# Kernel tuning notes

Hardware: AMD Instinct MI355X
Metric: run time of the kernel (lower is better)

Reference implementation:

```python
import jax, jax.numpy as jnp
import numpy as np

G = 4          # deformable groups (from offset_and_mask_dim = 3*4*3*3)
K = 9          # 3x3 kernel points
GN_GROUPS = 16 # GroupNorm groups as in DyHead


def conv2d(x, w, stride=1, pad=1, groups=1):
    return jax.lax.conv_general_dilated(
        x, w, (stride, stride), [(pad, pad), (pad, pad)],
        dimension_numbers=('NCHW', 'OIHW', 'NCHW'),
        feature_group_count=groups)


def dw_conv(x, w, scale, bias):
    # YOLO Conv with g=in_channels: depthwise 3x3 + folded BN + SiLU
    C = x.shape[1]
    y = conv2d(x, w, groups=C)
    y = y * scale[None, :, None, None] + bias[None, :, None, None]
    return y * jax.nn.sigmoid(y)


def offset_mask_conv(x, w, b):
    # Conv2d(C, 108, 3, padding=1, groups=4)
    return conv2d(x, w, groups=G) + b[None, :, None, None]


def split_offset_mask(om, use_softmax):
    # om: (N,108,H,W) -> offset (N,H,W,G,K,2) in pixels (dy,dx), mask (N,H,W,G,K)
    N, _, H, W = om.shape
    om = om.transpose(0, 2, 3, 1)
    offset = om[..., :2 * G * K].reshape(N, H, W, G, K, 2)
    m = om[..., 2 * G * K:].reshape(N, H, W, G, K)
    mask = jax.nn.softmax(m, axis=-1) if use_softmax else jax.nn.sigmoid(m)
    return offset, mask


def group_norm(x, gamma, beta, eps=1e-5):
    N, C, H, W = x.shape
    xg = x.reshape(N, GN_GROUPS, C // GN_GROUPS, H, W)
    mu = xg.mean((2, 3, 4), keepdims=True)
    var = xg.var((2, 3, 4), keepdims=True)
    xg = (xg - mu) * jax.lax.rsqrt(var + eps)
    return xg.reshape(N, C, H, W) * gamma[None, :, None, None] + beta[None, :, None, None]


def dcnv3_sample(x, offset, mask, stride):
    # DCNv3 core: group-wise deformable 3x3 bilinear sampling, zero padding.
    # x: (N,C,H,W); offset: (N,Ho,Wo,G,K,2); mask: (N,Ho,Wo,G,K) -> (N,C,Ho,Wo)
    N, C, H, W = x.shape
    Cg = C // G
    Ho, Wo = offset.shape[1], offset.shape[2]
    xg = x.transpose(0, 2, 3, 1).reshape(N, H, W, G, Cg)
    kk = jnp.arange(3, dtype=x.dtype) - 1.0
    ky = jnp.repeat(kk, 3)  # (9,)
    kx = jnp.tile(kk, 3)
    base_y = (jnp.arange(Ho, dtype=x.dtype) * stride)[None, :, None, None, None]
    base_x = (jnp.arange(Wo, dtype=x.dtype) * stride)[None, None, :, None, None]
    py = base_y + ky + offset[..., 0]   # (N,Ho,Wo,G,K)
    px = base_x + kx + offset[..., 1]
    y0 = jnp.floor(py)
    x0 = jnp.floor(px)
    wy = py - y0
    wx = px - x0
    y0i = y0.astype(jnp.int32)
    x0i = x0.astype(jnp.int32)
    n_idx = jnp.arange(N)[:, None, None, None, None]
    g_idx = jnp.arange(G)[None, None, None, :, None]
    acc = jnp.zeros((N, Ho, Wo, G, Cg), x.dtype)
    for dy in (0, 1):
        for dx in (0, 1):
            yi = y0i + dy
            xi = x0i + dx
            w = (wy if dy else 1.0 - wy) * (wx if dx else 1.0 - wx)
            valid = (yi >= 0) & (yi < H) & (xi >= 0) & (xi < W)
            w = w * valid.astype(x.dtype) * mask
            v = xg[n_idx, jnp.clip(yi, 0, H - 1), jnp.clip(xi, 0, W - 1), g_idx]  # (N,Ho,Wo,G,K,Cg)
            acc = acc + jnp.einsum('nhwgk,nhwgkc->nhwgc', w, v)
    return acc.reshape(N, Ho, Wo, C).transpose(0, 3, 1, 2)


def up_bilinear_ac(x, Ho, Wo):
    # bilinear, align_corners=True
    N, C, H, W = x.shape
    def coords(out, size):
        c = jnp.arange(out, dtype=jnp.float32) * ((size - 1) / max(out - 1, 1))
        i0 = jnp.floor(c).astype(jnp.int32)
        i1 = jnp.minimum(i0 + 1, size - 1)
        return i0, i1, (c - i0).astype(x.dtype)
    y0, y1, wy = coords(Ho, H)
    xc0, xc1, wx = coords(Wo, W)
    t = x[:, :, y0, :] * (1.0 - wy)[None, None, :, None] + x[:, :, y1, :] * wy[None, None, :, None]
    return t[:, :, :, xc0] * (1.0 - wx) + t[:, :, :, xc1] * wx


def scale_attn(f, w, b):
    # AdaptiveAvgPool2d(1) -> Conv 1x1 (C->1) -> ReLU -> HSigmoid(bias=3, divisor=6)
    y = f.mean((2, 3))                      # (N,C)
    a = jax.nn.relu(y @ w.T + b)            # (N,1)
    a = jnp.clip((a + 3.0) / 6.0, 0.0, 1.0)
    return f * a[:, :, None, None]


def dyrelu(f, w1, b1_, w2, b2_):
    # DyReLU with K2=True, use_bias=True, lambda_a=2, init_a=[1,0], init_b=[0,0]
    y = f.mean((2, 3))                      # (N,C)
    h = jax.nn.relu(y @ w1.T + b1_)
    z = jnp.clip(h @ w2.T + b2_ + 3.0, 0.0, 6.0) / 6.0  # h_sigmoid
    a1, b1, a2, b2 = jnp.split(z, 4, axis=1)
    a1 = (a1 - 0.5) * 2.0 + 1.0
    a2 = (a2 - 0.5) * 2.0
    b1 = b1 - 0.5
    b2 = b2 - 0.5
    bc = lambda t: t[:, :, None, None]
    return jnp.maximum(f * bc(a1) + bc(b1), f * bc(a2) + bc(b2))


def _forward(x0, x1, x2,
             dw_w_h, dw_s_h, dw_b_h, dw_w_m, dw_s_m, dw_b_m, dw_w_l, dw_s_l, dw_b_l,
             off_w, off_b,
             gn_g_h, gn_b_h, gn_g_m, gn_b_m, gn_g_l, gn_b_l,
             sa_w, sa_b, fc1_w, fc1_b, fc2_w, fc2_b):
    xs = [x0, x1, x2]
    outs = []
    for lvl in range(3):
        x = xs[lvl]
        mid_ = dw_conv(x, dw_w_m, dw_s_m, dw_b_m)
        off, msk = split_offset_mask(offset_mask_conv(mid_, off_w, off_b), use_softmax=False)
        mid_feat = group_norm(dcnv3_sample(x, off, msk, 1), gn_g_m, gn_b_m)
        sum_feat = scale_attn(mid_feat, sa_w, sa_b)
        n_lvls = 1
        if lvl > 0:
            xl = xs[lvl - 1]
            low_ = dw_conv(xl, dw_w_l, dw_s_l, dw_b_l)
            off, msk = split_offset_mask(offset_mask_conv(low_, off_w, off_b), use_softmax=True)
            off = off[:, ::2, ::2]   # stride-2 output grid
            msk = msk[:, ::2, ::2]
            low_feat = group_norm(dcnv3_sample(xl, off, msk, 2), gn_g_l, gn_b_l)
            sum_feat = sum_feat + scale_attn(low_feat, sa_w, sa_b)
            n_lvls += 1
        if lvl < 2:
            xh = xs[lvl + 1]
            high_ = dw_conv(xh, dw_w_h, dw_s_h, dw_b_h)
            off, msk = split_offset_mask(offset_mask_conv(high_, off_w, off_b), use_softmax=True)
            high_feat = group_norm(dcnv3_sample(xh, off, msk, 1), gn_g_h, gn_b_h)
            high_feat = up_bilinear_ac(high_feat, x.shape[2], x.shape[3])
            sum_feat = sum_feat + scale_attn(high_feat, sa_w, sa_b)
            n_lvls += 1
        outs.append(dyrelu(sum_feat / n_lvls, fc1_w, fc1_b, fc2_w, fc2_b))
    return tuple(outs)


def setup_inputs() -> dict:
    key = jax.random.key(0)
    ks = jax.random.split(key, 32)
    N, C = 4, 256
    f32 = jnp.float32
    nrm = lambda k, shape, s=1.0: jax.random.normal(k, shape, f32) * s
    inp = {
        'x0': nrm(ks[0], (N, C, 80, 80)),
        'x1': nrm(ks[1], (N, C, 40, 40)),
        'x2': nrm(ks[2], (N, C, 20, 20)),
        'dw_w_h': nrm(ks[3], (C, 1, 3, 3), 0.1),
        'dw_s_h': 1.0 + nrm(ks[4], (C,), 0.1),
        'dw_b_h': nrm(ks[5], (C,), 0.1),
        'dw_w_m': nrm(ks[6], (C, 1, 3, 3), 0.1),
        'dw_s_m': 1.0 + nrm(ks[7], (C,), 0.1),
        'dw_b_m': nrm(ks[8], (C,), 0.1),
        'dw_w_l': nrm(ks[9], (C, 1, 3, 3), 0.1),
        'dw_s_l': 1.0 + nrm(ks[10], (C,), 0.1),
        'dw_b_l': nrm(ks[11], (C,), 0.1),
        'off_w': nrm(ks[12], (108, C // G, 3, 3), 0.1),
        'off_b': nrm(ks[13], (108,), 0.1),
        'gn_g_h': 1.0 + nrm(ks[14], (C,), 0.1),
        'gn_b_h': nrm(ks[15], (C,), 0.1),
        'gn_g_m': 1.0 + nrm(ks[16], (C,), 0.1),
        'gn_b_m': nrm(ks[17], (C,), 0.1),
        'gn_g_l': 1.0 + nrm(ks[18], (C,), 0.1),
        'gn_b_l': nrm(ks[19], (C,), 0.1),
        'sa_w': nrm(ks[20], (1, C), 0.05),
        'sa_b': nrm(ks[21], (1,), 0.05),
        'fc1_w': nrm(ks[22], (C // 4, C), 0.05),
        'fc1_b': nrm(ks[23], (C // 4,), 0.05),
        'fc2_w': nrm(ks[24], (4 * C, C // 4), 0.05),
        'fc2_b': nrm(ks[25], (4 * C,), 0.1),
    }
    return inp


def reference(x0, x1, x2,
              dw_w_h, dw_s_h, dw_b_h, dw_w_m, dw_s_m, dw_b_m, dw_w_l, dw_s_l, dw_b_l,
              off_w, off_b,
              gn_g_h, gn_b_h, gn_g_m, gn_b_m, gn_g_l, gn_b_l,
              sa_w, sa_b, fc1_w, fc1_b, fc2_w, fc2_b):
    return _forward(x0, x1, x2,
                    dw_w_h, dw_s_h, dw_b_h, dw_w_m, dw_s_m, dw_b_m, dw_w_l, dw_s_l, dw_b_l,
                    off_w, off_b,
                    gn_g_h, gn_b_h, gn_g_m, gn_b_m, gn_g_l, gn_b_l,
                    sa_w, sa_b, fc1_w, fc1_b, fc2_w, fc2_b)
```

## Files before the change

kernel.cpp:

```cpp
#include <hip/hip_runtime.h>
#include <hip/hip_bf16.h>

#define C_ 256
#define G_ 4

typedef __attribute__((ext_vector_type(8))) short bf16x8;
typedef __attribute__((ext_vector_type(4))) float f32x4;

static __device__ __forceinline__ unsigned short f2bf(float x) {
    __hip_bfloat16 h = __float2bfloat16(x);
    return *(unsigned short*)&h;
}
static __device__ __forceinline__ float bf2f(unsigned short u) {
    return __uint_as_float((unsigned)u << 16);
}
static __device__ __forceinline__ float4 bf4(ushort4 u) {
    float4 r;
    r.x = bf2f(u.x);
    r.y = bf2f(u.y);
    r.z = bf2f(u.z);
    r.w = bf2f(u.w);
    return r;
}

static __device__ __forceinline__ float upw(int y, int Hr, int Hf, float sys) {
    float inv = 1.f / sys;
    int lo = max(0, (int)((y - 1) * inv) - 1);
    int hi = min(Hf - 1, (int)((y + 1) * inv) + 1);
    float w = 0.f;
    for (int o = lo; o <= hi; o++) {
        float sy = o * sys;
        int y0 = (int)sy;
        float fy = sy - y0;
        int y1 = min(y0 + 1, Hr - 1);
        if (y0 == y) w += 1.f - fy;
        if (y1 == y) w += fy;
    }
    return w;
}

__global__ void k_prep(const float* __restrict__ off_w, const float* __restrict__ dwh,
                       const float* __restrict__ dwm, const float* __restrict__ dwl,
                       unsigned short* __restrict__ wmf, float* __restrict__ dwt,
                       float* __restrict__ zeros, float* __restrict__ rep) {
    int i = blockIdx.x * 256 + threadIdx.x;
    const int NWM = 4 * 32 * 576;
    if (i < NWM) {
        int g = i / (32 * 576), rem = i % (32 * 576);
        int ol = rem / 576, kk = rem % 576;
        int tap = kk / 64, ic = kk % 64;
        float v = (ol < 27) ? off_w[((size_t)((g * 27 + ol) * 64 + ic)) * 9 + tap] : 0.f;
        wmf[i] = f2bf(v);
    }
    int j = i - NWM;
    if (j >= 0 && j < 3 * 2304) {
        int which = j / 2304, rem = j % 2304;
        int t = rem / 256, c = rem % 256;
        const float* src = (which == 0) ? dwh : (which == 1) ? dwm : dwl;
        dwt[j] = src[c * 9 + t];
    }
    int z = i - NWM - 3 * 2304;
    if (z >= 0 && z < 896) zeros[z] = 0.f;
    int z2 = z - 896;
    if (z2 >= 0 && z2 < 4 * 7168) rep[z2] = 0.f;
}

struct TrP {
    const float* x[3];
    unsigned short* xtb[3];
    int H[3];
    int W[3];
    int wtc[3];
    int blk[4];
};

__global__ __launch_bounds__(256) void k_transpose_b(TrP P) {
    __shared__ float tile[32][33];
    int b = blockIdx.x;
    int f = (b >= P.blk[1]) + (b >= P.blk[2]);
    int l = b - P.blk[f];
    int H = P.H[f], W = P.W[f], wtc = P.wtc[f];
    int nh = l / wtc, wtile = l - nh * wtc;
    int n = nh / H, h = nh % H;
    int w0 = wtile * 32, c0 = blockIdx.y * 32;
    const float* x = P.x[f];
    unsigned short* xtb = P.xtb[f];
    int tid = threadIdx.x;
    int i = tid / 32, j = tid % 32;
#pragma unroll
    for (int r = 0; r < 4; r++) {
        int c = c0 + i + r * 8;
        int w = w0 + j;
        tile[i + r * 8][j] = (w < W) ? x[((size_t)(n * C_ + c) * H + h) * W + w] : 0.f;
    }
    __syncthreads();
    int wj = tid >> 4, ci2 = (tid & 15) * 2;
#pragma unroll
    for (int r = 0; r < 2; r++) {
        int w = w0 + wj + r * 16;
        if (w < W) {
            ushort2 o;
            o.x = f2bf(tile[ci2][wj + r * 16]);
            o.y = f2bf(tile[ci2 + 1][wj + r * 16]);
            *(ushort2*)(xtb + ((size_t)(n * H + h) * W + w) * C_ + c0 + ci2) = o;
        }
    }
}

struct DwP {
    const unsigned short* xtb[7];
    unsigned short* out[7];
    const float* wdt[7];
    const float* sc[7];
    const float* bi[7];
    int H[7];
    int W[7];
    int blk[8];
};

__global__ __launch_bounds__(256) void k_dw_silu_b(DwP P) {
    int b = blockIdx.x;
    int f = (b >= P.blk[1]) + (b >= P.blk[2]) + (b >= P.blk[3]) + (b >= P.blk[4]) +
            (b >= P.blk[5]) + (b >= P.blk[6]);
    int H = P.H[f], W = P.W[f];
    const unsigned short* xtbf = P.xtb[f];
    unsigned short* outf = P.out[f];
    const float* wdt = P.wdt[f];
    int tid = threadIdx.x;
    int wv = tid >> 6, lane = tid & 63;
    int half = lane >> 5, l5 = lane & 31;
    int ch8 = l5 << 3;
    int pix = (b - P.blk[f]) * 8 + wv * 2 + half;
    int w = pix % W, h = (pix / W) % H, n = pix / (W * H);
    const float4 sA = *(const float4*)(P.sc[f] + ch8);
    const float4 sB = *(const float4*)(P.sc[f] + ch8 + 4);
    const float4 bA = *(const float4*)(P.bi[f] + ch8);
    const float4 bB = *(const float4*)(P.bi[f] + ch8 + 4);
    const unsigned short* xb = xtbf + (size_t)n * H * W * C_ + ch8;
    float4 accA = {0.f, 0.f, 0.f, 0.f}, accB = {0.f, 0.f, 0.f, 0.f};
#pragma unroll
    for (int t = 0; t < 9; t++) {
        int hh = h + t / 3 - 1, ww = w + t % 3 - 1;
        if (hh >= 0 && hh < H && ww >= 0 && ww < W) {
            bf16x8 xv = *(const bf16x8*)(xb + (size_t)(hh * W + ww) * C_);
            float4 wa = *(const float4*)(wdt + t * 256 + ch8);
            float4 wb = *(const float4*)(wdt + t * 256 + ch8 + 4);
            accA.x += wa.x * bf2f((unsigned short)xv[0]);
            accA.y += wa.y * bf2f((unsigned short)xv[1]);
            accA.z += wa.z * bf2f((unsigned short)xv[2]);
            accA.w += wa.w * bf2f((unsigned short)xv[3]);
            accB.x += wb.x * bf2f((unsigned short)xv[4]);
            accB.y += wb.y * bf2f((unsigned short)xv[5]);
            accB.z += wb.z * bf2f((unsigned short)xv[6]);
            accB.w += wb.w * bf2f((unsigned short)xv[7]);
        }
    }
    float y0 = accA.x * sA.x + bA.x, y1 = accA.y * sA.y + bA.y;
    float y2 = accA.z * sA.z + bA.z, y3 = accA.w * sA.w + bA.w;
    float y4 = accB.x * sB.x + bB.x, y5 = accB.y * sB.y + bB.y;
    float y6 = accB.z * sB.z + bB.z, y7 = accB.w * sB.w + bB.w;
    y0 = y0 / (1.f + __expf(-y0));
    y1 = y1 / (1.f + __expf(-y1));
    y2 = y2 / (1.f + __expf(-y2));
    y3 = y3 / (1.f + __expf(-y3));
    y4 = y4 / (1.f + __expf(-y4));
    y5 = y5 / (1.f + __expf(-y5));
    y6 = y6 / (1.f + __expf(-y6));
    y7 = y7 / (1.f + __expf(-y7));
    uint4 ov;
    ov.x = (unsigned)f2bf(y0) | ((unsigned)f2bf(y1) << 16);
    ov.y = (unsigned)f2bf(y2) | ((unsigned)f2bf(y3) << 16);
    ov.z = (unsigned)f2bf(y4) | ((unsigned)f2bf(y5) << 16);
    ov.w = (unsigned)f2bf(y6) | ((unsigned)f2bf(y7) << 16);
    *(uint4*)(outf + (size_t)pix * C_ + ch8) = ov;
}

struct OmP7 {
    const unsigned short* dwb[7];
    float* om[7];
    int Hs[7], Ws[7], Wo[7], HoWo[7];
    int ss[7];
    int ths[7], tws[7];
    int SR[7], SC[7], Msc[7];
    int nz[7], Mnz[7];
    int blk[8];
};

__global__ __launch_bounds__(256) void k_offmask_b(OmP7 P,
                                                   const unsigned short* __restrict__ wmf) {
    __shared__ __align__(16) char smem[22032];
    unsigned short* patch = (unsigned short*)smem;
    float* omv = (float*)smem;

    int tid = threadIdx.x;
    int wv = tid >> 6, lane = tid & 63;
    int n16 = lane & 15, q = lane >> 4;
    int b = blockIdx.x;
    int f = (b >= P.blk[1]) + (b >= P.blk[2]) + (b >= P.blk[3]) + (b >= P.blk[4]) +
            (b >= P.blk[5]) + (b >= P.blk[6]);
    int l = b - P.blk[f];
    int n = (l >> 2) & 3, g = l & 3;
    int tile = l >> 4;
    int nz = P.nz[f];
    int ty = (tile * P.Mnz[f]) >> 16;
    int tz = tile - ty * nz;
    int ss = P.ss[f], ths = P.ths[f], tws = P.tws[f];
    int TW = 1 << tws;
    int SR = P.SR[f], SC = P.SC[f], Msc = P.Msc[f];
    int NV = SR * SC;
    int Hs = P.Hs[f], Ws = P.Ws[f], Wo = P.Wo[f], HoWo = P.HoWo[f];
    int ho0 = ty << ths, wo0 = tz << tws;
    int hs0 = (ho0 << ss) - 1, ws0 = (wo0 << ss) - 1;
    const unsigned short* dwb = P.dwb[f];
    float* om = P.om[f];

    for (int idx = tid; idx < NV * 8; idx += 256) {
        int pp = idx >> 3;
        int c8 = (idx & 7) << 3;
        int pq = (pp * Msc) >> 16;
        int hh = hs0 + pq, ww = ws0 + (pp - pq * SC);
        uint4 v = {0u, 0u, 0u, 0u};
        if (hh >= 0 && hh < Hs && ww >= 0 && ww < Ws)
            v = *(const uint4*)(dwb + ((size_t)(n * Hs + hh) * Ws + ww) * C_ + g * 64 + c8);
        *(uint4*)(patch + pp * 72 + c8) = v;
    }
    __syncthreads();

    int bchan = q << 3;
    const unsigned short* wg = wmf + (size_t)g * 32 * 576;
    int TP = 1 << (ths + tws);
    int sc1 = SC, sc2 = SC * 2;

    if (TP == 64) {
        int p = wv * 16 + n16;
        int pr = p >> tws, pc = p & (TW - 1);
        int pixbase = (pr << ss) * SC + (pc << ss);
        f32x4 a0 = {0.f, 0.f, 0.f, 0.f}, a1 = {0.f, 0.f, 0.f, 0.f};
#pragma unroll
        for (int kk = 0; kk < 18; kk++) {
            int tap = kk >> 1;
            int ic0 = (kk & 1) << 5;
            int tr = tap / 3, tc = tap % 3;
            int ppix = pixbase + (tr == 0 ? 0 : (tr == 1 ? sc1 : sc2)) + tc;
            bf16x8 bb = *(const bf16x8*)(patch + ppix * 72 + ic0 + bchan);
            bf16x8 wa0 = *(const bf16x8*)(wg + (size_t)n16 * 576 + kk * 32 + bchan);
            bf16x8 wa1 = *(const bf16x8*)(wg + (size_t)(16 + n16) * 576 + kk * 32 + bchan);
            a0 = __builtin_amdgcn_mfma_f32_16x16x32_bf16(wa0, bb, a0, 0, 0, 0);
            a1 = __builtin_amdgcn_mfma_f32_16x16x32_bf16(wa1, bb, a1, 0, 0, 0);
        }
        __syncthreads();
#pragma unroll
        for (int r = 0; r < 4; r++) {
            int ol0 = q * 4 + r;
            omv[p * 28 + ol0] = a0[r];
            int ol1 = 16 + q * 4 + r;
            if (ol1 < 28) omv[p * 28 + ol1] = a1[r];
        }
    } else {
        int NT = TP >> 3;
        int t = wv;
        bool active = t < NT;
        int ntile = t >> 1, mtile = t & 1;
        int p = ntile * 16 + n16;
        int pr = p >> tws, pc = p & (TW - 1);
        int pixbase = (pr << ss) * SC + (pc << ss);
        f32x4 acc = {0.f, 0.f, 0.f, 0.f};
        if (active) {
#pragma unroll
            for (int kk = 0; kk < 18; kk++) {
                int tap = kk >> 1;
                int ic0 = (kk & 1) << 5;
                int tr = tap / 3, tc = tap % 3;
                int ppix = pixbase + (tr == 0 ? 0 : (tr == 1 ? sc1 : sc2)) + tc;
                bf16x8 bb = *(const bf16x8*)(patch + ppix * 72 + ic0 + bchan);
                bf16x8 wa = *(const bf16x8*)(wg + (size_t)(mtile * 16 + n16) * 576 +
                                             kk * 32 + bchan);
                acc = __builtin_amdgcn_mfma_f32_16x16x32_bf16(wa, bb, acc, 0, 0, 0);
            }
        }
        __syncthreads();
        if (active) {
#pragma unroll
            for (int r = 0; r < 4; r++) {
                int ol = mtile * 16 + q * 4 + r;
                if (ol < 28) omv[p * 28 + ol] = acc[r];
            }
        }
    }
    __syncthreads();

    float* omg = om + ((size_t)(g * 4 + n)) * HoWo * 28;
    for (int idx = tid; idx < TP * 7; idx += 256) {
        int p = (idx * 9363) >> 16;
        int c4 = idx - p * 7;
        int ho = ho0 + (p >> tws), wo = wo0 + (p & (TW - 1));
        int pixn = ho * Wo + wo;
        *(float4*)(omg + (size_t)pixn * 28 + c4 * 4) = *(float4*)(omv + p * 28 + c4 * 4);
    }
}

struct SmP {
    const unsigned short* xtb[7];
    const float* om[7];
    unsigned short* raw[7];
    float* stats[7];
    float* rsum[7];
    int Hs[7];
    int Ws[7];
    int Wo[7];
    int HoWo[7];
    int stride[7];
    int softmax[7];
    int up[7];
    int Hf[7];
    int Wf2[7];
    float sys[7];
    float sxs[7];
    int blk[8];
};

__global__ __launch_bounds__(256) void k_sample_b(SmP P, const float* __restrict__ bias) {
    int tid = threadIdx.x;
    int wv = tid >> 6, lane = tid & 63;
    int halfp = lane >> 5, l5 = lane & 31;
    int g = l5 >> 3;
    int ch8 = l5 << 3;
    int nb = gridDim.x;
    int per = nb >> 3, rem = nb & 7;
    int xcd = blockIdx.x & 7, bi = blockIdx.x >> 3;
    int logical = xcd * per + min(xcd, rem) + bi;
    int f = (logical >= P.blk[1]) + (logical >= P.blk[2]) + (logical >= P.blk[3]) +
            (logical >= P.blk[4]) + (logical >= P.blk[5]) + (logical >= P.blk[6]);
    const unsigned short* xtb = P.xtb[f];
    const float* om = P.om[f];
    unsigned short* raw = P.raw[f];
    float* stats = P.stats[f];
    float* rsum = P.rsum[f] + (blockIdx.x & 3) * 7168;
    int Hs = P.Hs[f], Ws = P.Ws[f], Wo = P.Wo[f], HoWo = P.HoWo[f];
    int stride = P.stride[f], softmax = P.softmax[f];
    int upf = P.up[f];
    int pix0 = (logical - P.blk[f]) * 8;
    int n = pix0 / HoWo;
    int pixn0 = pix0 - n * HoWo;

    __shared__ float lom[8 * 112];
    __shared__ float lb[108];
    __shared__ float sm[32][9];
    __shared__ float4 lw[288];
    __shared__ ushort4 li[288];
    __shared__ float lstat[32];
    __shared__ float lsum[8][256];
    __shared__ float wup[8];

    if (tid < 224) {
        int gc = tid / 56, r2 = tid % 56;
        int pp = r2 / 7, c4 = r2 % 7;
        float4 v = *(const float4*)(om + ((size_t)(gc * 4 + n) * HoWo + pixn0 + pp) * 28 +
                                    c4 * 4);
        ((float4*)lom)[pp * 28 + gc * 7 + c4] = v;
    }
    if (tid < 108) lb[tid] = bias[tid];
    if (tid < 32) lstat[tid] = 0.f;
    __syncthreads();

    if (tid < 32) {
        int pp = tid >> 2, gs = tid & 3;
        float mv[9];
#pragma unroll
        for (int k = 0; k < 9; k++) {
            int ch = 72 + gs * 9 + k;
            int gc = ch / 27;
            mv[k] = lom[pp * 112 + gc * 28 + (ch - gc * 27)] + lb[ch];
        }
        if (softmax) {
            float mx = -1e30f;
#pragma unroll
            for (int k = 0; k < 9; k++) mx = fmaxf(mx, mv[k]);
            float ssum = 0.f;
#pragma unroll
            for (int k = 0; k < 9; k++) {
                mv[k] = __expf(mv[k] - mx);
                ssum += mv[k];
            }
            float inv = 1.f / ssum;
#pragma unroll
            for (int k = 0; k < 9; k++) sm[tid][k] = mv[k] * inv;
        } else {
#pragma unroll
            for (int k = 0; k < 9; k++) sm[tid][k] = 1.f / (1.f + __expf(-mv[k]));
        }
    }
    if (tid < 8) {
        float w = 1.f;
        if (upf) {
            int Ho = HoWo / Wo;
            int pixn = pixn0 + tid;
            int ho = pixn / Wo, wo = pixn - ho * Wo;
            w = upw(ho, Ho, P.Hf[f], P.sys[f]) * upw(wo, Wo, P.Wf2[f], P.sxs[f]);
        }
        wup[tid] = w;
    }
    __syncthreads();

    for (int idx = tid; idx < 288; idx += 256) {
        int pg = idx / 9, k = idx % 9;
        int pp = pg >> 2, gs = pg & 3;
        int chy = gs * 18 + 2 * k, chx = chy + 1;
        int gcy = chy / 27, gcx = chx / 27;
        float oy = lom[pp * 112 + gcy * 28 + (chy - gcy * 27)] + lb[chy];
        float ox = lom[pp * 112 + gcx * 28 + (chx - gcx * 27)] + lb[chx];
        int pixn = pixn0 + pp;
        int ho = pixn / Wo, wo = pixn % Wo;
        float py = (float)(ho * stride + k / 3 - 1) + oy;
        float px = (float)(wo * stride + k % 3 - 1) + ox;
        float y0f = floorf(py), x0f = floorf(px);
        int y0 = (int)y0f, x0 = (int)x0f;
        float wy = py - y0f, wx = px - x0f;
        int y1 = y0 + 1, x1 = x0 + 1;
        float v0y = (y0 >= 0 && y0 < Hs) ? 1.f : 0.f;
        float v1y = (y1 >= 0 && y1 < Hs) ? 1.f : 0.f;
        float v0x = (x0 >= 0 && x0 < Ws) ? 1.f : 0.f;
        float v1x = (x1 >= 0 && x1 < Ws) ? 1.f : 0.f;
        int y0c = min(max(y0, 0), Hs - 1), y1c = min(max(y1, 0), Hs - 1);
        int x0c = min(max(x0, 0), Ws - 1), x1c = min(max(x1, 0), Ws - 1);
        float m_ = sm[pg][k];
        float4 w4;
        w4.x = (1.f - wy) * (1.f - wx) * v0y * v0x * m_;
        w4.y = (1.f - wy) * wx * v0y * v1x * m_;
        w4.z = wy * (1.f - wx) * v1y * v0x * m_;
        w4.w = wy * wx * v1y * v1x * m_;
// ... 185 lines not shown
__global__ __launch_bounds__(256) void k_store_b(StP P, const float* __restrict__ coef,
                                                 const float* __restrict__ af) {
    __shared__ float tile[64][65];
    int b = blockIdx.x;
    int f = (b >= P.blk[1]) + (b >= P.blk[2]);
    int l = b - P.blk[f];
    int npt = P.npt[f], HW = P.HW[f], Wf = P.Wf[f], nf = P.nf[f];
    int n = l / (npt * 4);
    int r_ = l - n * (npt * 4);
    int pt = r_ >> 2;
    int c0 = (r_ & 3) * 64;
    float* out = P.out[f];
    const float* coefL = coef + f * 4096;
    const float* afL = af + f * 16;
    int tid = threadIdx.x;
    int lane16 = tid & 15, prow = tid >> 4;
    int ch4 = c0 + lane16 * 4;
    int gg = ch4 >> 4;
    float a0 = afL[n * 4 + 0], a1f = afL[n * 4 + 1], a2f = afL[n * 4 + 2];
    float4 ca1 = *(const float4*)(coefL + n * 1024 + 0 + ch4);
    float4 cb1 = *(const float4*)(coefL + n * 1024 + 256 + ch4);
    float4 ca2 = *(const float4*)(coefL + n * 1024 + 512 + ch4);
    float4 cb2 = *(const float4*)(coefL + n * 1024 + 768 + ch4);

    StF sA = P.ft[f][0], sB = P.ft[f][1], sC = P.ft[f][2];
    auto mkgb = [&](const StF& s, float4& ga, float4& be) {
        float s1 = s.stats[(n * 16 + gg) * 2], s2 = s.stats[(n * 16 + gg) * 2 + 1];
        float mu = s1 / s.cnt;
        float var = s2 / s.cnt - mu * mu;
        float rs = rsqrtf(var + 1e-5f);
        float4 gm = *(const float4*)(s.gamma + ch4);
        float4 bt = *(const float4*)(s.beta + ch4);
        ga.x = gm.x * rs; be.x = bt.x - mu * ga.x;
        ga.y = gm.y * rs; be.y = bt.y - mu * ga.y;
        ga.z = gm.z * rs; be.z = bt.z - mu * ga.z;
        ga.w = gm.w * rs; be.w = bt.w - mu * ga.w;
    };
    float4 gaA, beA, gaB, beB, gaC = {0, 0, 0, 0}, beC = {0, 0, 0, 0};
    mkgb(sA, gaA, beA);
    mkgb(sB, gaB, beB);
    if (nf > 2) mkgb(sC, gaC, beC);

    auto rdf = [&](const StF& s, int p) -> float4 {
        if (!s.up)
            return bf4(*(const ushort4*)(s.raw + ((size_t)n * HW + p) * C_ + ch4));
        int ho = p / Wf, wo = p - ho * Wf;
        float sy = ho * s.sys, sx = wo * s.sxs;
        int y0 = (int)sy, x0 = (int)sx;
        float fy = sy - y0, fx = sx - x0;
        int y1 = min(y0 + 1, s.Hr - 1), x1 = min(x0 + 1, s.Wr - 1);
        const unsigned short* rb = s.raw + (size_t)n * s.Hr * s.Wr * C_ + ch4;
        float4 v00 = bf4(*(const ushort4*)(rb + (size_t)(y0 * s.Wr + x0) * C_));
        float4 v01 = bf4(*(const ushort4*)(rb + (size_t)(y0 * s.Wr + x1) * C_));
        float4 v10 = bf4(*(const ushort4*)(rb + (size_t)(y1 * s.Wr + x0) * C_));
        float4 v11 = bf4(*(const ushort4*)(rb + (size_t)(y1 * s.Wr + x1) * C_));
        float4 v;
        v.x = (v00.x * (1.f - fy) + v10.x * fy) * (1.f - fx) + (v01.x * (1.f - fy) + v11.x * fy) * fx;
        v.y = (v00.y * (1.f - fy) + v10.y * fy) * (1.f - fx) + (v01.y * (1.f - fy) + v11.y * fy) * fx;
        v.z = (v00.z * (1.f - fy) + v10.z * fy) * (1.f - fx) + (v01.z * (1.f - fy) + v11.z * fy) * fx;
        v.w = (v00.w * (1.f - fy) + v10.w * fy) * (1.f - fx) + (v01.w * (1.f - fy) + v11.w * fy) * fx;
        return v;
    };

#pragma unroll
    for (int pass = 0; pass < 4; pass++) {
        int px = pass * 16 + prow;
        int p = pt * 64 + px;
        if (p < HW) {
            float4 vA = rdf(sA, p);
            float4 fv;
            fv.x = (vA.x * gaA.x + beA.x) * a0;
            fv.y = (vA.y * gaA.y + beA.y) * a0;
            fv.z = (vA.z * gaA.z + beA.z) * a0;
            fv.w = (vA.w * gaA.w + beA.w) * a0;
            float4 vB = rdf(sB, p);
            fv.x += (vB.x * gaB.x + beB.x) * a1f;
            fv.y += (vB.y * gaB.y + beB.y) * a1f;
            fv.z += (vB.z * gaB.z + beB.z) * a1f;
            fv.w += (vB.w * gaB.w + beB.w) * a1f;
            if (nf > 2) {
                float4 vC = rdf(sC, p);
                fv.x += (vC.x * gaC.x + beC.x) * a2f;
                fv.y += (vC.y * gaC.y + beC.y) * a2f;
                fv.z += (vC.z * gaC.z + beC.z) * a2f;
                fv.w += (vC.w * gaC.w + beC.w) * a2f;
            }
            int cr = lane16 * 4;
            tile[cr + 0][px] = fmaxf(fv.x * ca1.x + cb1.x, fv.x * ca2.x + cb2.x);
            tile[cr + 1][px] = fmaxf(fv.y * ca1.y + cb1.y, fv.y * ca2.y + cb2.y);
            tile[cr + 2][px] = fmaxf(fv.z * ca1.z + cb1.z, fv.z * ca2.z + cb2.z);
            tile[cr + 3][px] = fmaxf(fv.w * ca1.w + cb1.w, fv.w * ca2.w + cb2.w);
        }
    }
    __syncthreads();
#pragma unroll
    for (int wp = 0; wp < 4; wp++) {
        int row = wp * 16 + (tid >> 4);
        int px4 = (tid & 15) * 4;
        int p = pt * 64 + px4;
        if (p < HW) {
            float4 r;
            r.x = tile[row][px4 + 0];
            r.y = tile[row][px4 + 1];
            r.z = tile[row][px4 + 2];
            r.w = tile[row][px4 + 3];
            *(float4*)(out + (size_t)(n * C_ + c0 + row) * HW + p) = r;
        }
    }
}

extern "C" void kernel_launch(void* const* d_in, const int* in_sizes, int n_in,
                              void* d_out, int out_size, void* d_ws, size_t ws_size,
                              hipStream_t stream) {
    (void)in_sizes; (void)n_in; (void)out_size; (void)ws_size;
    const float* x0 = (const float*)d_in[0];
    const float* x1 = (const float*)d_in[1];
    const float* x2 = (const float*)d_in[2];
    const float* dw_w_h = (const float*)d_in[3];
    const float* dw_s_h = (const float*)d_in[4];
    const float* dw_b_h = (const float*)d_in[5];
    const float* dw_w_m = (const float*)d_in[6];
    const float* dw_s_m = (const float*)d_in[7];
    const float* dw_b_m = (const float*)d_in[8];
    const float* dw_w_l = (const float*)d_in[9];
    const float* dw_s_l = (const float*)d_in[10];
    const float* dw_b_l = (const float*)d_in[11];
    const float* off_w = (const float*)d_in[12];
    const float* off_b = (const float*)d_in[13];
    const float* gn_g_h = (const float*)d_in[14];
    const float* gn_b_h = (const float*)d_in[15];
    const float* gn_g_m = (const float*)d_in[16];
    const float* gn_b_m = (const float*)d_in[17];
    const float* gn_g_l = (const float*)d_in[18];
    const float* gn_b_l = (const float*)d_in[19];
    const float* sa_w = (const float*)d_in[20];
    const float* sa_b = (const float*)d_in[21];
    const float* fc1_w = (const float*)d_in[22];
    const float* fc1_b = (const float*)d_in[23];
    const float* fc2_w = (const float*)d_in[24];
    const float* fc2_b = (const float*)d_in[25];

    float* ws = (float*)d_ws;
    unsigned short* XTB0 = (unsigned short*)(ws + 0);
    unsigned short* XTB1 = (unsigned short*)(ws + 3276800);
    unsigned short* XTB2 = (unsigned short*)(ws + 4096000);
    float* SH = ws + 4300800;
    float* FINA = ws + 10854400;
    float* FINB = ws + 17408000;
    float* FINC = ws + 23961600;
    float* WMF = ws + 25600000;
    float* DWT = ws + 25636864;
    float* STATS = ws + 25643776;

    unsigned short* SHB = (unsigned short*)SH;
    unsigned short* FINAB = (unsigned short*)FINA;
    unsigned short* WMFB = (unsigned short*)WMF;

    float* out0 = (float*)d_out;
    float* out1 = out0 + 6553600;
    float* out2 = out0 + 8192000;

    float* OM_l0mid = out0;
    float* OM_l0high = out0 + 2867200;
    float* OM_l1mid = out0 + 3584000;
    float* OM_l1low = out0 + 4300800;
    float* OM_l1high = out1;
    float* OM_l2mid = out1 + 179200;
    float* OM_l2low = out1 + 358400;

    unsigned short* RAW_l0mid = (unsigned short*)SH;
    unsigned short* RAW_l0high = (unsigned short*)FINC;
    unsigned short* RAW_l1mid = (unsigned short*)FINB;
    unsigned short* RAW_l1low = (unsigned short*)(FINB + 1638400);
    unsigned short* RAW_l1high = (unsigned short*)(FINB + 3276800);
    unsigned short* RAW_l2mid = (unsigned short*)(FINB + 3686400);
    unsigned short* RAW_l2low = (unsigned short*)(FINB + 4096000);
    float* REP = FINB + 4505600;
    float* COEF = FINA;
    float* AF = FINA + 12288;

    const float SYS_L0H = (float)(39.0 / 79.0);
    const float SYS_L1H = (float)(19.0 / 39.0);

    k_prep<<<(4 * 32 * 576 + 6912 + 896 + 28672 + 255) / 256, 256, 0, stream>>>(
        off_w, dw_w_h, dw_w_m, dw_w_l, WMFB, DWT, STATS, REP);

    {
        TrP tp{};
        tp.x[0] = x0; tp.xtb[0] = XTB0; tp.H[0] = 80; tp.W[0] = 80; tp.wtc[0] = 3;
        tp.x[1] = x1; tp.xtb[1] = XTB1; tp.H[1] = 40; tp.W[1] = 40; tp.wtc[1] = 2;
        tp.x[2] = x2; tp.xtb[2] = XTB2; tp.H[2] = 20; tp.W[2] = 20; tp.wtc[2] = 1;
        tp.blk[0] = 0; tp.blk[1] = 960; tp.blk[2] = 1280; tp.blk[3] = 1360;
        k_transpose_b<<<dim3(1360, 8), 256, 0, stream>>>(tp);
    }

    unsigned short* DWB_x0mid = SHB;
    unsigned short* DWB_x0low = SHB + 6553600;
    unsigned short* DWB_x1high = FINAB;
    unsigned short* DWB_x1mid = FINAB + 1638400;
    unsigned short* DWB_x1low = FINAB + 3276800;
    unsigned short* DWB_x2high = FINAB + 4915200;
    unsigned short* DWB_x2mid = FINAB + 5324800;

    {
        DwP dp{};
        dp.xtb[0] = XTB0; dp.out[0] = DWB_x0mid;  dp.wdt[0] = DWT + 1 * 2304;
        dp.sc[0] = dw_s_m; dp.bi[0] = dw_b_m; dp.H[0] = 80; dp.W[0] = 80;
        dp.xtb[1] = XTB0; dp.out[1] = DWB_x0low;  dp.wdt[1] = DWT + 2 * 2304;
        dp.sc[1] = dw_s_l; dp.bi[1] = dw_b_l; dp.H[1] = 80; dp.W[1] = 80;
        dp.xtb[2] = XTB1; dp.out[2] = DWB_x1high; dp.wdt[2] = DWT + 0 * 2304;
        dp.sc[2] = dw_s_h; dp.bi[2] = dw_b_h; dp.H[2] = 40; dp.W[2] = 40;
        dp.xtb[3] = XTB1; dp.out[3] = DWB_x1mid;  dp.wdt[3] = DWT + 1 * 2304;
        dp.sc[3] = dw_s_m; dp.bi[3] = dw_b_m; dp.H[3] = 40; dp.W[3] = 40;
        dp.xtb[4] = XTB1; dp.out[4] = DWB_x1low;  dp.wdt[4] = DWT + 2 * 2304;
        dp.sc[4] = dw_s_l; dp.bi[4] = dw_b_l; dp.H[4] = 40; dp.W[4] = 40;
        dp.xtb[5] = XTB2; dp.out[5] = DWB_x2high; dp.wdt[5] = DWT + 0 * 2304;
        dp.sc[5] = dw_s_h; dp.bi[5] = dw_b_h; dp.H[5] = 20; dp.W[5] = 20;
        dp.xtb[6] = XTB2; dp.out[6] = DWB_x2mid;  dp.wdt[6] = DWT + 1 * 2304;
        dp.sc[6] = dw_s_m; dp.bi[6] = dw_b_m; dp.H[6] = 20; dp.W[6] = 20;
        dp.blk[0] = 0;    dp.blk[1] = 3200; dp.blk[2] = 6400; dp.blk[3] = 7200;
        dp.blk[4] = 8000; dp.blk[5] = 8800; dp.blk[6] = 9000; dp.blk[7] = 9200;
        k_dw_silu_b<<<9200, 256, 0, stream>>>(dp);
    }

    {
        OmP7 op{};
        auto setf = [&](int i, const unsigned short* dwb, float* om, int Hs, int Ws,
                        int Wo, int HoWo, int ss, int ths, int tws, int SR, int SC,
                        int nz) {
            op.dwb[i] = dwb; op.om[i] = om;
            op.Hs[i] = Hs; op.Ws[i] = Ws; op.Wo[i] = Wo; op.HoWo[i] = HoWo;
            op.ss[i] = ss; op.ths[i] = ths; op.tws[i] = tws;
            op.SR[i] = SR; op.SC[i] = SC; op.Msc[i] = (65536 + SC - 1) / SC;
            op.nz[i] = nz; op.Mnz[i] = (65536 + nz - 1) / nz;
        };
        setf(0, DWB_x0mid,  OM_l0mid,  80, 80, 80, 6400, 0, 3, 3, 10, 10, 10);
        setf(1, DWB_x1high, OM_l0high, 40, 40, 40, 1600, 0, 2, 3, 6,  10, 5);
        setf(2, DWB_x1mid,  OM_l1mid,  40, 40, 40, 1600, 0, 2, 3, 6,  10, 5);
        setf(3, DWB_x0low,  OM_l1low,  80, 80, 40, 1600, 1, 2, 3, 9,  17, 5);
        setf(4, DWB_x2high, OM_l1high, 20, 20, 20, 400,  0, 2, 2, 6,  6,  5);
        setf(5, DWB_x2mid,  OM_l2mid,  20, 20, 20, 400,  0, 2, 2, 6,  6,  5);
        setf(6, DWB_x1low,  OM_l2low,  40, 40, 20, 400,  1, 2, 2, 9,  9,  5);
        op.blk[0] = 0;    op.blk[1] = 1600; op.blk[2] = 2400; op.blk[3] = 3200;
        op.blk[4] = 4000; op.blk[5] = 4400; op.blk[6] = 4800; op.blk[7] = 5200;
        k_offmask_b<<<5200, 256, 0, stream>>>(op, WMFB);
    }

    {
        SmP sp{};
        auto setf = [&](int i, const unsigned short* xtb, const float* om,
                        unsigned short* raw, int slot, int Hs, int Ws, int Wo, int HoWo,
                        int stride, int softmax, int up, int Hf, int Wf2, float sys,
                        float sxs) {
            sp.xtb[i] = xtb; sp.om[i] = om; sp.raw[i] = raw;
            sp.stats[i] = STATS + slot * 128;
            sp.rsum[i] = REP + slot * 1024;
            sp.Hs[i] = Hs; sp.Ws[i] = Ws; sp.Wo[i] = Wo; sp.HoWo[i] = HoWo;
            sp.stride[i] = stride; sp.softmax[i] = softmax;
            sp.up[i] = up; sp.Hf[i] = Hf; sp.Wf2[i] = Wf2;
            sp.sys[i] = sys; sp.sxs[i] = sxs;
        };
        setf(0, XTB0, OM_l0mid,  RAW_l0mid,  0, 80, 80, 80, 6400, 1, 0, 0, 80, 80, 1.f, 1.f);
        setf(1, XTB1, OM_l0high, RAW_l0high, 1, 40, 40, 40, 1600, 1, 1, 1, 80, 80, SYS_L0H, SYS_L0H);
        setf(2, XTB1, OM_l1mid,  RAW_l1mid,  2, 40, 40, 40, 1600, 1, 0, 0, 40, 40, 1.f, 1.f);
        setf(3, XTB0, OM_l1low,  RAW_l1low,  3, 80, 80, 40, 1600, 2, 1, 0, 40, 40, 1.f, 1.f);
        setf(4, XTB2, OM_l1high, RAW_l1high, 4, 20, 20, 20, 400,  1, 1, 1, 40, 40, SYS_L1H, SYS_L1H);
        setf(5, XTB2, OM_l2mid,  RAW_l2mid,  5, 20, 20, 20, 400,  1, 0, 0, 20, 20, 1.f, 1.f);
        setf(6, XTB1, OM_l2low,  RAW_l2low,  6, 40, 40, 20, 400,  2, 1, 0, 20, 20, 1.f, 1.f);
        sp.blk[0] = 0;    sp.blk[1] = 3200; sp.blk[2] = 4000; sp.blk[3] = 4800;
        sp.blk[4] = 5600; sp.blk[5] = 5800; sp.blk[6] = 6000; sp.blk[7] = 6200;
        k_sample_b<<<6200, 256, 0, stream>>>(sp, off_b);
    }

    {
        CfP cp{};
        cp.nf[0] = 2; cp.inv_nl[0] = 0.5f;      cp.inv_hw[0] = 1.f / 6400.f;
        cp.nf[1] = 3; cp.inv_nl[1] = 1.f / 3.f; cp.inv_hw[1] = 1.f / 1600.f;
        cp.nf[2] = 2; cp.inv_nl[2] = 0.5f;      cp.inv_hw[2] = 1.f / 400.f;
        cp.ft[0][0] = {REP + 0 * 1024, STATS + 0 * 128, gn_g_m, gn_b_m, 102400.f};
        cp.ft[0][1] = {REP + 1 * 1024, STATS + 1 * 128, gn_g_h, gn_b_h, 25600.f};
        cp.ft[1][0] = {REP + 2 * 1024, STATS + 2 * 128, gn_g_m, gn_b_m, 25600.f};
        cp.ft[1][1] = {REP + 3 * 1024, STATS + 3 * 128, gn_g_l, gn_b_l, 25600.f};
        cp.ft[1][2] = {REP + 4 * 1024, STATS + 4 * 128, gn_g_h, gn_b_h, 6400.f};
        cp.ft[2][0] = {REP + 5 * 1024, STATS + 5 * 128, gn_g_m, gn_b_m, 6400.f};
        cp.ft[2][1] = {REP + 6 * 1024, STATS + 6 * 128, gn_g_l, gn_b_l, 6400.f};
        k_coef_b<<<12, 256, 0, stream>>>(cp, sa_w, sa_b, fc1_w, fc1_b, fc2_w, fc2_b,
                                         COEF, AF);
    }

    {
        StP st{};
        st.out[0] = out0; st.nf[0] = 2; st.HW[0] = 6400; st.Wf[0] = 80; st.npt[0] = 100;
        st.out[1] = out1; st.nf[1] = 3; st.HW[1] = 1600; st.Wf[1] = 40; st.npt[1] = 25;
        st.out[2] = out2; st.nf[2] = 2; st.HW[2] = 400;  st.Wf[2] = 20; st.npt[2] = 7;
        st.ft[0][0] = {RAW_l0mid,  STATS + 0 * 128, gn_g_m, gn_b_m, 102400.f, 0, 80, 80, 1.f, 1.f};
        st.ft[0][1] = {RAW_l0high, STATS + 1 * 128, gn_g_h, gn_b_h, 25600.f,  1, 40, 40, SYS_L0H, SYS_L0H};
        st.ft[1][0] = {RAW_l1mid,  STATS + 2 * 128, gn_g_m, gn_b_m, 25600.f,  0, 40, 40, 1.f, 1.f};
        st.ft[1][1] = {RAW_l1low,  STATS + 3 * 128, gn_g_l, gn_b_l, 25600.f,  0, 40, 40, 1.f, 1.f};
        st.ft[1][2] = {RAW_l1high, STATS + 4 * 128, gn_g_h, gn_b_h, 6400.f,   1, 20, 20, SYS_L1H, SYS_L1H};
        st.ft[2][0] = {RAW_l2mid,  STATS + 5 * 128, gn_g_m, gn_b_m, 6400.f,   0, 20, 20, 1.f, 1.f};
        st.ft[2][1] = {RAW_l2low,  STATS + 6 * 128, gn_g_l, gn_b_l, 6400.f,   0, 20, 20, 1.f, 1.f};
        st.blk[0] = 0; st.blk[1] = 1600; st.blk[2] = 2000; st.blk[3] = 2112;
        k_store_b<<<2112, 256, 0, stream>>>(st, COEF, AF);
    }
}
```

Baseline: 358.6 us.

## Fuse depthwise conv+SiLU into offset/mask conv via shared-memory halo patch

Removes the standalone depthwise conv + BN + SiLU kernel and its bf16 intermediate buffers. Each offset/mask block now loads a wider halo patch of the transposed input into shared memory and computes the depthwise output for its patch there, then runs the MFMA grouped conv on it. The work is split into two template instantiations, one for the stride-1 levels and one for the stride-2 levels, each sized for its patch. This saves a global write and read of seven intermediate maps, but recomputes the depthwise conv on overlapping halos and uses more shared memory per block, which could lower occupancy.

```diff
diff --git a/kernel.cpp b/kernel.cpp
--- a/kernel.cpp
+++ b/kernel.cpp
@@ -107,97 +107,31 @@
     }
 }
 
-struct DwP {
-    const unsigned short* xtb[7];
-    unsigned short* out[7];
-    const float* wdt[7];
-    const float* sc[7];
-    const float* bi[7];
-    int H[7];
-    int W[7];
-    int blk[8];
+struct OdP {
+    const unsigned short* xtb[5];
+    float* om[5];
+    const float* wdt[5];
+    const float* sc[5];
+    const float* bi[5];
+    int Hs[5], Ws[5], Wo[5], HoWo[5];
+    int ss[5], ths[5], tws[5];
+    int SR[5], SC[5], Msc[5], XC[5], Mxc[5];
+    int nz[5], Mnz[5];
+    int blk[6];
 };
 
-__global__ __launch_bounds__(256) void k_dw_silu_b(DwP P) {
-    int b = blockIdx.x;
-    int f = (b >= P.blk[1]) + (b >= P.blk[2]) + (b >= P.blk[3]) + (b >= P.blk[4]) +
-            (b >= P.blk[5]) + (b >= P.blk[6]);
-    int H = P.H[f], W = P.W[f];
-    const unsigned short* xtbf = P.xtb[f];
-    unsigned short* outf = P.out[f];
-    const float* wdt = P.wdt[f];
-    int tid = threadIdx.x;
-    int wv = tid >> 6, lane = tid & 63;
-    int half = lane >> 5, l5 = lane & 31;
-    int ch8 = l5 << 3;
-    int pix = (b - P.blk[f]) * 8 + wv * 2 + half;
-    int w = pix % W, h = (pix / W) % H, n = pix / (W * H);
-    const float4 sA = *(const float4*)(P.sc[f] + ch8);
-    const float4 sB = *(const float4*)(P.sc[f] + ch8 + 4);
-    const float4 bA = *(const float4*)(P.bi[f] + ch8);
-    const float4 bB = *(const float4*)(P.bi[f] + ch8 + 4);
-    const unsigned short* xb = xtbf + (size_t)n * H * W * C_ + ch8;
-    float4 accA = {0.f, 0.f, 0.f, 0.f}, accB = {0.f, 0.f, 0.f, 0.f};
-#pragma unroll
-    for (int t = 0; t < 9; t++) {
-        int hh = h + t / 3 - 1, ww = w + t % 3 - 1;
-        if (hh >= 0 && hh < H && ww >= 0 && ww < W) {
-            bf16x8 xv = *(const bf16x8*)(xb + (size_t)(hh * W + ww) * C_);
-            float4 wa = *(const float4*)(wdt + t * 256 + ch8);
-            float4 wb = *(const float4*)(wdt + t * 256 + ch8 + 4);
-            accA.x += wa.x * bf2f((unsigned short)xv[0]);
-            accA.y += wa.y * bf2f((unsigned short)xv[1]);
-            accA.z += wa.z * bf2f((unsigned short)xv[2]);
-            accA.w += wa.w * bf2f((unsigned short)xv[3]);
-            accB.x += wb.x * bf2f((unsigned short)xv[4]);
-            accB.y += wb.y * bf2f((unsigned short)xv[5]);
-            accB.z += wb.z * bf2f((unsigned short)xv[6]);
-            accB.w += wb.w * bf2f((unsigned short)xv[7]);
-        }
-    }
-    float y0 = accA.x * sA.x + bA.x, y1 = accA.y * sA.y + bA.y;
-    float y2 = accA.z * sA.z + bA.z, y3 = accA.w * sA.w + bA.w;
-    float y4 = accB.x * sB.x + bB.x, y5 = accB.y * sB.y + bB.y;
-    float y6 = accB.z * sB.z + bB.z, y7 = accB.w * sB.w + bB.w;
-    y0 = y0 / (1.f + __expf(-y0));
-    y1 = y1 / (1.f + __expf(-y1));
-    y2 = y2 / (1.f + __expf(-y2));
-    y3 = y3 / (1.f + __expf(-y3));
-    y4 = y4 / (1.f + __expf(-y4));
-    y5 = y5 / (1.f + __expf(-y5));
-    y6 = y6 / (1.f + __expf(-y6));
-    y7 = y7 / (1.f + __expf(-y7));
-    uint4 ov;
-    ov.x = (unsigned)f2bf(y0) | ((unsigned)f2bf(y1) << 16);
-    ov.y = (unsigned)f2bf(y2) | ((unsigned)f2bf(y3) << 16);
-    ov.z = (unsigned)f2bf(y4) | ((unsigned)f2bf(y5) << 16);
-    ov.w = (unsigned)f2bf(y6) | ((unsigned)f2bf(y7) << 16);
-    *(uint4*)(outf + (size_t)pix * C_ + ch8) = ov;
-}
-
-struct OmP7 {
-    const unsigned short* dwb[7];
-    float* om[7];
-    int Hs[7], Ws[7], Wo[7], HoWo[7];
-    int ss[7];
-    int ths[7], tws[7];
-    int SR[7], SC[7], Msc[7];
-    int nz[7], Mnz[7];
-    int blk[8];
-};
-
-__global__ __launch_bounds__(256) void k_offmask_b(OmP7 P,
-                                                   const unsigned short* __restrict__ wmf) {
-    __shared__ __align__(16) char smem[22032];
-    unsigned short* patch = (unsigned short*)smem;
-    float* omv = (float*)smem;
+template <int XPX, int PPX>
+__global__ __launch_bounds__(256) void k_offdw_b(OdP P,
+                                                 const unsigned short* __restrict__ wmf) {
+    __shared__ __align__(16) unsigned short xpatch[XPX * 72];
+    __shared__ __align__(16) unsigned short patch[PPX * 72];
+    float* omv = (float*)xpatch;
 
     int tid = threadIdx.x;
     int wv = tid >> 6, lane = tid & 63;
     int n16 = lane & 15, q = lane >> 4;
     int b = blockIdx.x;
-    int f = (b >= P.blk[1]) + (b >= P.blk[2]) + (b >= P.blk[3]) + (b >= P.blk[4]) +
-            (b >= P.blk[5]) + (b >= P.blk[6]);
+    int f = (b >= P.blk[1]) + (b >= P.blk[2]) + (b >= P.blk[3]) + (b >= P.blk[4]);
     int l = b - P.blk[f];
     int n = (l >> 2) & 3, g = l & 3;
     int tile = l >> 4;
@@ -207,22 +141,74 @@
     int ss = P.ss[f], ths = P.ths[f], tws = P.tws[f];
     int TW = 1 << tws;
     int SR = P.SR[f], SC = P.SC[f], Msc = P.Msc[f];
+    int XC = P.XC[f], Mxc = P.Mxc[f];
+    int XNV = (SR + 2) * XC;
     int NV = SR * SC;
     int Hs = P.Hs[f], Ws = P.Ws[f], Wo = P.Wo[f], HoWo = P.HoWo[f];
     int ho0 = ty << ths, wo0 = tz << tws;
     int hs0 = (ho0 << ss) - 1, ws0 = (wo0 << ss) - 1;
-    const unsigned short* dwb = P.dwb[f];
+    const unsigned short* xtb = P.xtb[f] + (size_t)n * Hs * Ws * C_ + g * 64;
     float* om = P.om[f];
+    const float* wdt = P.wdt[f] + g * 64;
+    const float* scp = P.sc[f] + g * 64;
+    const float* bip = P.bi[f] + g * 64;
+
+    for (int idx = tid; idx < XNV * 8; idx += 256) {
+        int pp = idx >> 3;
+        int c8 = (idx & 7) << 3;
+        int pq = (pp * Mxc) >> 16;
+        int hh = hs0 - 1 + pq, ww = ws0 - 1 + (pp - pq * XC);
+        uint4 v = {0u, 0u, 0u, 0u};
+        if (hh >= 0 && hh < Hs && ww >= 0 && ww < Ws)
+            v = *(const uint4*)(xtb + ((size_t)hh * Ws + ww) * C_ + c8);
+        *(uint4*)(xpatch + pp * 72 + c8) = v;
+    }
+    __syncthreads();
 
     for (int idx = tid; idx < NV * 8; idx += 256) {
         int pp = idx >> 3;
         int c8 = (idx & 7) << 3;
         int pq = (pp * Msc) >> 16;
-        int hh = hs0 + pq, ww = ws0 + (pp - pq * SC);
-        uint4 v = {0u, 0u, 0u, 0u};
-        if (hh >= 0 && hh < Hs && ww >= 0 && ww < Ws)
-            v = *(const uint4*)(dwb + ((size_t)(n * Hs + hh) * Ws + ww) * C_ + g * 64 + c8);
-        *(uint4*)(patch + pp * 72 + c8) = v;
+        int pr = pq, pc = pp - pq * SC;
+        int hh = hs0 + pr, ww = ws0 + pc;
+        uint4 ov = {0u, 0u, 0u, 0u};
+        if (hh >= 0 && hh < Hs && ww >= 0 && ww < Ws) {
+            float4 accA = {0.f, 0.f, 0.f, 0.f}, accB = {0.f, 0.f, 0.f, 0.f};
+#pragma unroll
+            for (int t = 0; t < 9; t++) {
+                int xr = pr + t / 3, xc = pc + t % 3;
+                bf16x8 xv = *(const bf16x8*)(xpatch + (xr * XC + xc) * 72 + c8);
+                float4 wa = *(const float4*)(wdt + t * 256 + c8);
+                float4 wb = *(const float4*)(wdt + t * 256 + c8 + 4);
+                accA.x += wa.x * bf2f((unsigned short)xv[0]);
+                accA.y += wa.y * bf2f((unsigned short)xv[1]);
+                accA.z += wa.z * bf2f((unsigned short)xv[2]);
+                accA.w += wa.w * bf2f((unsigned short)xv[3]);
+                accB.x += wb.x * bf2f((unsigned short)xv[4]);
+                accB.y += wb.y * bf2f((unsigned short)xv[5]);
+                accB.z += wb.z * bf2f((unsigned short)xv[6]);
+                accB.w += wb.w * bf2f((unsigned short)xv[7]);
+            }
+            float4 sa = *(const float4*)(scp + c8), sb = *(const float4*)(scp + c8 + 4);
+            float4 ba = *(const float4*)(bip + c8), bb = *(const float4*)(bip + c8 + 4);
+            float y0 = accA.x * sa.x + ba.x, y1 = accA.y * sa.y + ba.y;
+            float y2 = accA.z * sa.z + ba.z, y3 = accA.w * sa.w + ba.w;
+            float y4 = accB.x * sb.x + bb.x, y5 = accB.y * sb.y + bb.y;
+            float y6 = accB.z * sb.z + bb.z, y7 = accB.w * sb.w + bb.w;
+            y0 = y0 / (1.f + __expf(-y0));
+            y1 = y1 / (1.f + __expf(-y1));
+            y2 = y2 / (1.f + __expf(-y2));
+            y3 = y3 / (1.f + __expf(-y3));
+            y4 = y4 / (1.f + __expf(-y4));
+            y5 = y5 / (1.f + __expf(-y5));
+            y6 = y6 / (1.f + __expf(-y6));
+            y7 = y7 / (1.f + __expf(-y7));
+            ov.x = (unsigned)f2bf(y0) | ((unsigned)f2bf(y1) << 16);
+            ov.y = (unsigned)f2bf(y2) | ((unsigned)f2bf(y3) << 16);
+            ov.z = (unsigned)f2bf(y4) | ((unsigned)f2bf(y5) << 16);
+            ov.w = (unsigned)f2bf(y6) | ((unsigned)f2bf(y7) << 16);
+        }
+        *(uint4*)(patch + pp * 72 + c8) = ov;
     }
     __syncthreads();
 
@@ -242,11 +228,11 @@
             int ic0 = (kk & 1) << 5;
             int tr = tap / 3, tc = tap % 3;
             int ppix = pixbase + (tr == 0 ? 0 : (tr == 1 ? sc1 : sc2)) + tc;
-            bf16x8 bb = *(const bf16x8*)(patch + ppix * 72 + ic0 + bchan);
+            bf16x8 bbv = *(const bf16x8*)(patch + ppix * 72 + ic0 + bchan);
             bf16x8 wa0 = *(const bf16x8*)(wg + (size_t)n16 * 576 + kk * 32 + bchan);
             bf16x8 wa1 = *(const bf16x8*)(wg + (size_t)(16 + n16) * 576 + kk * 32 + bchan);
-            a0 = __builtin_amdgcn_mfma_f32_16x16x32_bf16(wa0, bb, a0, 0, 0, 0);
-            a1 = __builtin_amdgcn_mfma_f32_16x16x32_bf16(wa1, bb, a1, 0, 0, 0);
+            a0 = __builtin_amdgcn_mfma_f32_16x16x32_bf16(wa0, bbv, a0, 0, 0, 0);
+            a1 = __builtin_amdgcn_mfma_f32_16x16x32_bf16(wa1, bbv, a1, 0, 0, 0);
         }
         __syncthreads();
 #pragma unroll
@@ -272,10 +258,10 @@
                 int ic0 = (kk & 1) << 5;
                 int tr = tap / 3, tc = tap % 3;
                 int ppix = pixbase + (tr == 0 ? 0 : (tr == 1 ? sc1 : sc2)) + tc;
-                bf16x8 bb = *(const bf16x8*)(patch + ppix * 72 + ic0 + bchan);
+                bf16x8 bbv = *(const bf16x8*)(patch + ppix * 72 + ic0 + bchan);
                 bf16x8 wa = *(const bf16x8*)(wg + (size_t)(mtile * 16 + n16) * 576 +
                                              kk * 32 + bchan);
-                acc = __builtin_amdgcn_mfma_f32_16x16x32_bf16(wa, bb, acc, 0, 0, 0);
+                acc = __builtin_amdgcn_mfma_f32_16x16x32_bf16(wa, bbv, acc, 0, 0, 0);
             }
         }
         __syncthreads();
@@ -767,8 +753,6 @@
     float* DWT = ws + 25636864;
     float* STATS = ws + 25643776;
 
-    unsigned short* SHB = (unsigned short*)SH;
-    unsigned short* FINAB = (unsigned short*)FINA;
     unsigned short* WMFB = (unsigned short*)WMF;
 
     float* out0 = (float*)d_out;
@@ -809,56 +793,42 @@
         k_transpose_b<<<dim3(1360, 8), 256, 0, stream>>>(tp);
     }
 
-    unsigned short* DWB_x0mid = SHB;
-    unsigned short* DWB_x0low = SHB + 6553600;
-    unsigned short* DWB_x1high = FINAB;
-    unsigned short* DWB_x1mid = FINAB + 1638400;
-    unsigned short* DWB_x1low = FINAB + 3276800;
-    unsigned short* DWB_x2high = FINAB + 4915200;
-    unsigned short* DWB_x2mid = FINAB + 5324800;
+    auto setod = [&](OdP& op, int i, const unsigned short* xtb, float* om,
+                     const float* wdt, const float* sc, const float* bi, int Hs, int Ws,
+                     int Wo, int HoWo, int ss, int ths, int tws, int SR, int SC, int nz) {
+        op.xtb[i] = xtb; op.om[i] = om; op.wdt[i] = wdt; op.sc[i] = sc; op.bi[i] = bi;
+        op.Hs[i] = Hs; op.Ws[i] = Ws; op.Wo[i] = Wo; op.HoWo[i] = HoWo;
+        op.ss[i] = ss; op.ths[i] = ths; op.tws[i] = tws;
+        op.SR[i] = SR; op.SC[i] = SC; op.Msc[i] = (65536 + SC - 1) / SC;
+        op.XC[i] = SC + 2; op.Mxc[i] = (65536 + SC + 1) / (SC + 2);
+        op.nz[i] = nz; op.Mnz[i] = (65536 + nz - 1) / nz;
+    };
 
     {
-        DwP dp{};
-        dp.xtb[0] = XTB0; dp.out[0] = DWB_x0mid;  dp.wdt[0] = DWT + 1 * 2304;
-        dp.sc[0] = dw_s_m; dp.bi[0] = dw_b_m; dp.H[0] = 80; dp.W[0] = 80;
-        dp.xtb[1] = XTB0; dp.out[1] = DWB_x0low;  dp.wdt[1] = DWT + 2 * 2304;
-        dp.sc[1] = dw_s_l; dp.bi[1] = dw_b_l; dp.H[1] = 80; dp.W[1] = 80;
-        dp.xtb[2] = XTB1; dp.out[2] = DWB_x1high; dp.wdt[2] = DWT + 0 * 2304;
-        dp.sc[2] = dw_s_h; dp.bi[2] = dw_b_h; dp.H[2] = 40; dp.W[2] = 40;
-        dp.xtb[3] = XTB1; dp.out[3] = DWB_x1mid;  dp.wdt[3] = DWT + 1 * 2304;
-        dp.sc[3] = dw_s_m; dp.bi[3] = dw_b_m; dp.H[3] = 40; dp.W[3] = 40;
-        dp.xtb[4] = XTB1; dp.out[4] = DWB_x1low;  dp.wdt[4] = DWT + 2 * 2304;
-        dp.sc[4] = dw_s_l; dp.bi[4] = dw_b_l; dp.H[4] = 40; dp.W[4] = 40;
-        dp.xtb[5] = XTB2; dp.out[5] = DWB_x2high; dp.wdt[5] = DWT + 0 * 2304;
-        dp.sc[5] = dw_s_h; dp.bi[5] = dw_b_h; dp.H[5] = 20; dp.W[5] = 20;
-        dp.xtb[6] = XTB2; dp.out[6] = DWB_x2mid;  dp.wdt[6] = DWT + 1 * 2304;
-        dp.sc[6] = dw_s_m; dp.bi[6] = dw_b_m; dp.H[6] = 20; dp.W[6] = 20;
-        dp.blk[0] = 0;    dp.blk[1] = 3200; dp.blk[2] = 6400; dp.blk[3] = 7200;
-        dp.blk[4] = 8000; dp.blk[5] = 8800; dp.blk[6] = 9000; dp.blk[7] = 9200;
-        k_dw_silu_b<<<9200, 256, 0, stream>>>(dp);
-    }
-
+        OdP op{};
+        setod(op, 0, XTB0, OM_l0mid,  DWT + 1 * 2304, dw_s_m, dw_b_m, 80, 80, 80, 6400,
+              0, 3, 3, 10, 10, 10);
+        setod(op, 1, XTB1, OM_l0high, DWT + 0 * 2304, dw_s_h, dw_b_h, 40, 40, 40, 1600,
+              0, 2, 3, 6, 10, 5);
+        setod(op, 2, XTB1, OM_l1mid,  DWT + 1 * 2304, dw_s_m, dw_b_m, 40, 40, 40, 1600,
+              0, 2, 3, 6, 10, 5);
+        setod(op, 3, XTB2, OM_l1high, DWT + 0 * 2304, dw_s_h, dw_b_h, 20, 20, 20, 400,
+              0, 2, 2, 6, 6, 5);
+        setod(op, 4, XTB2, OM_l2mid,  DWT + 1 * 2304, dw_s_m, dw_b_m, 20, 20, 20, 400,
+              0, 2, 2, 6, 6, 5);
+        op.blk[0] = 0; op.blk[1] = 1600; op.blk[2] = 2400; op.blk[3] = 3200;
+        op.blk[4] = 3600; op.blk[5] = 4000;
+        k_offdw_b<144, 100><<<4000, 256, 0, stream>>>(op, WMFB);
+    }
     {
-        OmP7 op{};
-        auto setf = [&](int i, const unsigned short* dwb, float* om, int Hs, int Ws,
-                        int Wo, int HoWo, int ss, int ths, int tws, int SR, int SC,
-                        int nz) {
-            op.dwb[i] = dwb; op.om[i] = om;
-            op.Hs[i] = Hs; op.Ws[i] = Ws; op.Wo[i] = Wo; op.HoWo[i] = HoWo;
-            op.ss[i] = ss; op.ths[i] = ths; op.tws[i] = tws;
-            op.SR[i] = SR; op.SC[i] = SC; op.Msc[i] = (65536 + SC - 1) / SC;
-            op.nz[i] = nz; op.Mnz[i] = (65536 + nz - 1) / nz;
-        };
-        setf(0, DWB_x0mid,  OM_l0mid,  80, 80, 80, 6400, 0, 3, 3, 10, 10, 10);
-        setf(1, DWB_x1high, OM_l0high, 40, 40, 40, 1600, 0, 2, 3, 6,  10, 5);
-        setf(2, DWB_x1mid,  OM_l1mid,  40, 40, 40, 1600, 0, 2, 3, 6,  10, 5);
-        setf(3, DWB_x0low,  OM_l1low,  80, 80, 40, 1600, 1, 2, 3, 9,  17, 5);
-        setf(4, DWB_x2high, OM_l1high, 20, 20, 20, 400,  0, 2, 2, 6,  6,  5);
-        setf(5, DWB_x2mid,  OM_l2mid,  20, 20, 20, 400,  0, 2, 2, 6,  6,  5);
-        setf(6, DWB_x1low,  OM_l2low,  40, 40, 20, 400,  1, 2, 2, 9,  9,  5);
-        op.blk[0] = 0;    op.blk[1] = 1600; op.blk[2] = 2400; op.blk[3] = 3200;
-        op.blk[4] = 4000; op.blk[5] = 4400; op.blk[6] = 4800; op.blk[7] = 5200;
-        k_offmask_b<<<5200, 256, 0, stream>>>(op, WMFB);
+        OdP op{};
+        setod(op, 0, XTB0, OM_l1low, DWT + 2 * 2304, dw_s_l, dw_b_l, 80, 80, 40, 1600,
+              1, 2, 3, 9, 17, 5);
+        setod(op, 1, XTB1, OM_l2low, DWT + 2 * 2304, dw_s_l, dw_b_l, 40, 40, 20, 400,
+              1, 2, 2, 9, 9, 5);
+        op.blk[0] = 0; op.blk[1] = 800; op.blk[2] = 1200; op.blk[3] = 1200;
+        op.blk[4] = 1200; op.blk[5] = 1200;
+        k_offdw_b<209, 153><<<1200, 256, 0, stream>>>(op, WMFB);
     }
 
     {
```

New measurement: 364.4 us. About the same (+1.6%).
